# Optimization experiments

Measured on AMD Instinct MI355X. Metric: run time of the kernel, lower is better.

## Reference

```python
import jax, jax.numpy as jnp
import numpy as np

B, Q, K = 4, 1024, 2048
QDIM, MDIM, EDIM, H = 1024, 1024, 1024, 16
HD = EDIM // H

def setup_inputs() -> dict:
    key = jax.random.key(0)
    ks = jax.random.split(key, 7)
    s = lambda d: (1.0 / np.sqrt(d))
    return {
        'query': jax.random.normal(ks[0], (B, Q, QDIM), jnp.float32),
        'memory': jax.random.normal(ks[1], (B, K, MDIM), jnp.float32),
        'bias': jax.random.normal(ks[2], (B, K), jnp.float32),
        'Wq': jax.random.normal(ks[3], (QDIM, EDIM), jnp.float32) * s(QDIM),
        'Wk': jax.random.normal(ks[4], (MDIM, EDIM), jnp.float32) * s(MDIM),
        'Wv': jax.random.normal(ks[5], (MDIM, EDIM), jnp.float32) * s(MDIM),
        'Wo': jax.random.normal(ks[6], (EDIM, EDIM), jnp.float32) * s(EDIM),
    }

def reference(query, memory, bias, Wq, Wk, Wv, Wo):
    scale = HD ** -0.5
    # projections -> [B, H, Q/K, HD]
    q = (query @ Wq).reshape(B, Q, H, HD).transpose(0, 2, 1, 3)
    k = (memory @ Wk).reshape(B, K, H, HD).transpose(0, 2, 1, 3)
    v = (memory @ Wv).reshape(B, K, H, HD).transpose(0, 2, 1, 3)
    scores = jnp.einsum('bhqd,bhkd->bhqk', q, k) * scale
    scores = scores + bias[:, None, None, :]
    weights = jax.nn.softmax(scores, axis=-1)
    out = jnp.einsum('bhqk,bhkd->bhqd', weights, v)
    out = out.transpose(0, 2, 1, 3).reshape(B, Q, EDIM)
    return out @ Wo
```

## Files before the change

### kernel.cpp

```cpp
#include <hip/hip_runtime.h>
#include <cstdint>
#include <cstddef>

typedef unsigned short u16;
typedef __attribute__((ext_vector_type(8))) short bf16x8;
typedef __attribute__((ext_vector_type(4))) short bf16x4;
typedef __attribute__((ext_vector_type(4))) float f32x4;

#define B_  4
#define Q_  1024
#define K_  2048
#define E_  1024
#define H_  16
#define HD_ 64
#define LOG2E 1.4426950408889634f
#define M0_  16.0f

__device__ inline u16 f2bf(float f) {
  union { float f; uint32_t u; } x; x.f = f;
  return (u16)((x.u + 0x7fffu + ((x.u >> 16) & 1u)) >> 16);
}

__device__ inline short bfc(float f) {
  __bf16 h = (__bf16)f;
  return __builtin_bit_cast(short, h);
}

__device__ inline void gload16(const u16* g, u16* l) {
  __builtin_amdgcn_global_load_lds((const __attribute__((address_space(1))) void*)g,
                                   (__attribute__((address_space(3))) void*)l, 16, 0, 0);
}

#define NQ8 (B_ * Q_ * E_ / 8)
#define NM8 (B_ * K_ * E_ / 8)
#define NBI (B_ * K_)
#define NPREP ((NQ8 + NM8 + NBI) / 256)
__global__ __launch_bounds__(256) void prep_all(const float* __restrict__ query,
                                                const float* __restrict__ memory,
                                                const float* __restrict__ bias,
                                                const float* W0, const float* W1,
                                                const float* W2, const float* W3,
                                                u16* __restrict__ qb,
                                                u16* __restrict__ mb,
                                                float* __restrict__ bias2,
                                                u16* T0, u16* T1, u16* T2, u16* T3) {
  __shared__ float t[64][65];
  int bid = blockIdx.x;
  if (bid < NPREP) {
    int i = bid * 256 + threadIdx.x;
    const float* src;
    u16* dst;
    if (i < NQ8) {
      src = query + (size_t)i * 8; dst = qb + (size_t)i * 8;
    } else if (i < NQ8 + NM8) {
      int j = i - NQ8;
      src = memory + (size_t)j * 8; dst = mb + (size_t)j * 8;
    } else {
      int j = i - (NQ8 + NM8);
      if (j < NBI) bias2[j] = bias[j] * LOG2E - M0_;
      return;
    }
    float4 a = *reinterpret_cast<const float4*>(src);
    float4 b = *reinterpret_cast<const float4*>(src + 4);
    union { u16 u[8]; uint4 v; } r;
    r.u[0] = f2bf(a.x); r.u[1] = f2bf(a.y); r.u[2] = f2bf(a.z); r.u[3] = f2bf(a.w);
    r.u[4] = f2bf(b.x); r.u[5] = f2bf(b.y); r.u[6] = f2bf(b.z); r.u[7] = f2bf(b.w);
    *reinterpret_cast<uint4*>(dst) = r.v;
  } else {
    int tb = bid - NPREP;
    int z = tb >> 8, xy = tb & 255;
    const float* W; u16* T;
    switch (z) {
      case 0: W = W0; T = T0; break;
      case 1: W = W1; T = T1; break;
      case 2: W = W2; T = T2; break;
      default: W = W3; T = T3; break;
    }
    int k0 = (xy & 15) * 64, n0 = (xy >> 4) * 64;
    int r = threadIdx.x >> 6, c = threadIdx.x & 63;
#pragma unroll
    for (int i = 0; i < 16; ++i)
      t[r + i * 4][c] = W[(size_t)(k0 + r + i * 4) * E_ + n0 + c];
    __syncthreads();
#pragma unroll
    for (int i = 0; i < 16; ++i)
      T[(size_t)(n0 + r + i * 4) * E_ + k0 + c] = f2bf(t[c][r + i * 4]);
  }
}

template <int MODE>
__device__ __forceinline__ void gemm_body(const u16* __restrict__ A,
                                          const u16* __restrict__ Bt,
                                          void* __restrict__ C,
                                          int M, int N, int Kc, int bx, int by,
                                          u16* As, u16* Bs) {
  const int tid = threadIdx.x;
  const int w = tid >> 6, l = tid & 63;
  const int wr = w >> 1, wc = w & 1;
  const int lr = l & 15, lg = l >> 4;
  const int m0 = bx * 128, n0 = by * 128;
  const int xk = (lr & 7) * 8;

  f32x4 acc[4][4];
#pragma unroll
  for (int mt = 0; mt < 4; ++mt)
#pragma unroll
    for (int nt = 0; nt < 4; ++nt)
      acc[mt][nt] = (f32x4){0.f, 0.f, 0.f, 0.f};

  for (int k0 = 0; k0 < Kc; k0 += 64) {
    __syncthreads();
#pragma unroll
    for (int r = 0; r < 4; ++r) {
      int e = (tid + r * 256) * 8;
      int row = e >> 6, col = e & 63;
      int sc = col ^ ((row & 7) * 8);
      gload16(A  + (size_t)(m0 + row) * Kc + k0 + sc, &As[e]);
      gload16(Bt + (size_t)(n0 + row) * Kc + k0 + sc, &Bs[e]);
    }
    __syncthreads();

#pragma unroll
    for (int ks = 0; ks < 2; ++ks) {
      bf16x8 a[4], b[4];
#pragma unroll
      for (int mt = 0; mt < 4; ++mt) {
        int row = wr * 64 + mt * 16 + lr;
        a[mt] = *reinterpret_cast<const bf16x8*>(&As[row * 64 + ((ks * 32 + lg * 8) ^ xk)]);
      }
#pragma unroll
      for (int nt = 0; nt < 4; ++nt) {
        int row = wc * 64 + nt * 16 + lr;
        b[nt] = *reinterpret_cast<const bf16x8*>(&Bs[row * 64 + ((ks * 32 + lg * 8) ^ xk)]);
      }
#pragma unroll
      for (int mt = 0; mt < 4; ++mt)
#pragma unroll
        for (int nt = 0; nt < 4; ++nt)
          acc[mt][nt] = __builtin_amdgcn_mfma_f32_16x16x32_bf16(a[mt], b[nt], acc[mt][nt], 0, 0, 0);
    }
  }

#pragma unroll
  for (int mt = 0; mt < 4; ++mt) {
#pragma unroll
    for (int nt = 0; nt < 4; ++nt) {
      int col = n0 + wc * 64 + nt * 16 + lr;
#pragma unroll
      for (int j = 0; j < 4; ++j) {
        int row = m0 + wr * 64 + mt * 16 + lg * 4 + j;
        float v = acc[mt][nt][j];
        if (MODE == 0) {
          ((float*)C)[(size_t)row * N + col] = v;
        } else if (MODE == 1) {
          ((u16*)C)[(size_t)row * N + col] = f2bf(v);
        } else if (MODE == 3) {
          ((u16*)C)[(size_t)row * N + col] = f2bf(v * (0.125f * LOG2E));
        } else {
          ((u16*)C)[((size_t)((col >> 11) * 16 + (row >> 6)) * 64 + (row & 63)) * 2048 + (col & 2047)] = f2bf(v);
        }
      }
    }
  }
}

__global__ __launch_bounds__(256) void gemm_out(const u16* __restrict__ A,
                                                const u16* __restrict__ Bt,
                                                void* __restrict__ C,
                                                int M, int N, int Kc) {
  __shared__ u16 As[128 * 64];
  __shared__ u16 Bs[128 * 64];
  int d = blockIdx.x;
  int bid = (d & 7) * 32 + (d >> 3);
  gemm_body<0>(A, Bt, C, M, N, Kc, bid >> 3, bid & 7, As, Bs);
}

__global__ __launch_bounds__(256) void proj_fused(const u16* __restrict__ qb,
                                                  const u16* __restrict__ mb,
                                                  const u16* __restrict__ wqt,
                                                  const u16* __restrict__ wkt,
                                                  const u16* __restrict__ wvt,
                                                  u16* __restrict__ qproj,
                                                  u16* __restrict__ kproj,
                                                  u16* __restrict__ vt) {
  __shared__ u16 As[128 * 64];
  __shared__ u16 Bs[128 * 64];
  int d = blockIdx.x;
  int bid = (d & 7) * 160 + (d >> 3);
  if (bid < 256) {
    gemm_body<3>(qb, wqt, qproj, B_ * Q_, E_, E_, bid >> 3, bid & 7, As, Bs);
  } else if (bid < 768) {
    int i = bid - 256;
    gemm_body<1>(mb, wkt, kproj, B_ * K_, E_, E_, i >> 3, i & 7, As, Bs);
  } else {
    int i = bid - 768;
    gemm_body<2>(wvt, mb, vt, E_, B_ * K_, E_, i & 7, i >> 3, As, Bs);
  }
}

__global__ __launch_bounds__(256, 4) void attn_kernel(const u16* __restrict__ qp,
                                                      const u16* __restrict__ kp,
                                                      const u16* __restrict__ vT,
                                                      const float* __restrict__ bias2,
                                                      u16* __restrict__ out) {
  __shared__ uint4 lds4[2048];
  char* ldsb = (char*)lds4;

  const int blk = blockIdx.x;
  const int hg = blk & 63, qt = blk >> 6;
  const int b = hg >> 4, h = hg & 15;
  const int tid = threadIdx.x;
  const int w = tid >> 6, l = tid & 63;
  const int lr = l & 15, lg = l >> 4;

  bf16x8 qfrag[2];
#pragma unroll
  for (int ks = 0; ks < 2; ++ks)
    qfrag[ks] = *reinterpret_cast<const bf16x8*>(
        qp + (size_t)(b * Q_ + qt * 64 + w * 16 + lr) * E_ + h * 64 + ks * 32 + lg * 8);

  f32x4 O[4];
  f32x4 Osum = (f32x4){0.f, 0.f, 0.f, 0.f};
#pragma unroll
  for (int ht = 0; ht < 4; ++ht) O[ht] = (f32x4){0.f, 0.f, 0.f, 0.f};
  const float* bias_b = bias2 + (size_t)b * K_;
  const u16* kbase = kp + (size_t)b * K_ * E_ + h * 64;
  const u16* vbase = vT + (size_t)(b * H_ + h) * HD_ * K_;

  const bf16x4 ones = {(short)0x3F80, (short)0x3F80, (short)0x3F80, (short)0x3F80};

  const int xk = (lr & 7) * 8;
  int kofs0 = lr * 128 + (((lg * 8) ^ xk) << 1);
  int kofs1 = lr * 128 + ((((32 + lg * 8)) ^ xk) << 1);
  int vofs[4];
#pragma unroll
  for (int ct = 0; ct < 4; ++ct)
    vofs[ct] = 16384 + lr * 128 + ((((ct * 16 + lg * 4)) ^ xk) << 1);

  const int e0 = tid * 8, e1 = e0 + 2048;
  const int r0 = e0 >> 6, r1 = e1 >> 6;
  const int sc0 = (e0 & 63) ^ ((r0 & 7) * 8);
  const int sc1 = (e1 & 63) ^ ((r1 & 7) * 8);

  gload16(kbase + (size_t)r0 * E_ + sc0, (u16*)(ldsb + tid * 16));
  gload16(kbase + (size_t)r1 * E_ + sc1, (u16*)(ldsb + 4096 + tid * 16));
  gload16(vbase + (size_t)r0 * K_ + sc0, (u16*)(ldsb + 16384 + tid * 16));
  gload16(vbase + (size_t)r1 * K_ + sc1, (u16*)(ldsb + 16384 + 4096 + tid * 16));
  __syncthreads();

  const int NT = K_ / 64;
  for (int t = 0; t < NT; ++t) {
    if (t + 1 < NT) {
      const int nb = ((t & 1) ^ 1) * 8192;
      int kk0 = (t + 1) * 64;
      gload16(kbase + (size_t)(kk0 + r0) * E_ + sc0, (u16*)(ldsb + nb + tid * 16));
      gload16(kbase + (size_t)(kk0 + r1) * E_ + sc1, (u16*)(ldsb + nb + 4096 + tid * 16));
      gload16(vbase + (size_t)r0 * K_ + kk0 + sc0, (u16*)(ldsb + 16384 + nb + tid * 16));
      gload16(vbase + (size_t)r1 * K_ + kk0 + sc1, (u16*)(ldsb + 16384 + nb + 4096 + tid * 16));
    }

    const float* bt = bias_b + t * 64;
    f32x4 S[4];
    __builtin_amdgcn_s_setprio(1);
#pragma unroll
    for (int ct = 0; ct < 4; ++ct) {
      bf16x8 kb0 = *reinterpret_cast<const bf16x8*>(ldsb + kofs0 + ct * 2048);
      bf16x8 kb1 = *reinterpret_cast<const bf16x8*>(ldsb + kofs1 + ct * 2048);
      float4 bv = *reinterpret_cast<const float4*>(&bt[ct * 16 + lg * 4]);
      f32x4 s; s[0] = bv.x; s[1] = bv.y; s[2] = bv.z; s[3] = bv.w;
      s = __builtin_amdgcn_mfma_f32_16x16x32_bf16(kb0, qfrag[0], s, 0, 0, 0);
      s = __builtin_amdgcn_mfma_f32_16x16x32_bf16(kb1, qfrag[1], s, 0, 0, 0);
      S[ct] = s;
    }
    __builtin_amdgcn_s_setprio(0);

    bf16x4 pf[4];
#pragma unroll
    for (int ct = 0; ct < 4; ++ct) {
      pf[ct][0] = bfc(exp2f(S[ct][0]));
      pf[ct][1] = bfc(exp2f(S[ct][1]));
      pf[ct][2] = bfc(exp2f(S[ct][2]));
      pf[ct][3] = bfc(exp2f(S[ct][3]));
    }

    __builtin_amdgcn_s_setprio(1);
#pragma unroll
    for (int ct = 0; ct < 4; ++ct) {
#pragma unroll
      for (int ht = 0; ht < 4; ++ht) {
        bf16x4 vb = *reinterpret_cast<const bf16x4*>(ldsb + vofs[ct] + ht * 2048);
        O[ht] = __builtin_amdgcn_mfma_f32_16x16x16bf16_1k(pf[ct], vb, O[ht], 0, 0, 0);
      }
      Osum = __builtin_amdgcn_mfma_f32_16x16x16bf16_1k(pf[ct], ones, Osum, 0, 0, 0);
    }
    __builtin_amdgcn_s_setprio(0);

    kofs0 ^= 8192; kofs1 ^= 8192;
#pragma unroll
    for (int ct = 0; ct < 4; ++ct) vofs[ct] ^= 8192;
    __syncthreads();
  }

#pragma unroll
  for (int j = 0; j < 4; ++j) {
    float inv = 1.f / Osum[j];
    int row = b * Q_ + qt * 64 + w * 16 + lg * 4 + j;
#pragma unroll
    for (int ht = 0; ht < 4; ++ht)
      out[(size_t)row * E_ + h * 64 + ht * 16 + lr] = (u16)bfc(O[ht][j] * inv);
  }
}

extern "C" void kernel_launch(void* const* d_in, const int* in_sizes, int n_in,
                              void* d_out, int out_size, void* d_ws, size_t ws_size,
                              hipStream_t stream) {
  const float* query  = (const float*)d_in[0];
  const float* memory = (const float*)d_in[1];
  const float* bias   = (const float*)d_in[2];
  const float* Wq     = (const float*)d_in[3];
  const float* Wk     = (const float*)d_in[4];
  const float* Wv     = (const float*)d_in[5];
  const float* Wo     = (const float*)d_in[6];
  float* out = (float*)d_out;

  char* p = (char*)d_ws;
  u16* qb    = (u16*)p; p += (size_t)B_ * Q_ * E_ * 2;
  u16* mb    = (u16*)p; p += (size_t)B_ * K_ * E_ * 2;
  u16* wqt   = (u16*)p; p += (size_t)E_ * E_ * 2;
  u16* wkt   = (u16*)p; p += (size_t)E_ * E_ * 2;
  u16* wvt   = (u16*)p; p += (size_t)E_ * E_ * 2;
  u16* wot   = (u16*)p; p += (size_t)E_ * E_ * 2;
  u16* qproj = (u16*)p; p += (size_t)B_ * Q_ * E_ * 2;
  u16* kproj = (u16*)p; p += (size_t)B_ * K_ * E_ * 2;
  u16* vt    = (u16*)p; p += (size_t)B_ * K_ * E_ * 2;
  u16* attn  = (u16*)p; p += (size_t)B_ * Q_ * E_ * 2;
  float* bias2 = (float*)p; p += (size_t)B_ * K_ * 4;

  prep_all<<<NPREP + 1024, 256, 0, stream>>>(query, memory, bias, Wq, Wk, Wv, Wo,
                                             qb, mb, bias2, wqt, wkt, wvt, wot);

  proj_fused<<<1280, 256, 0, stream>>>(qb, mb, wqt, wkt, wvt, qproj, kproj, vt);

  attn_kernel<<<B_ * H_ * (Q_ / 64), 256, 0, stream>>>(qproj, kproj, vt, bias2, attn);

  gemm_out<<<256, 256, 0, stream>>>(attn, wot, out, B_ * Q_, E_, E_);
}
```

Baseline: 164.2 us.

## Double-buffer projection GEMM LDS tiles with K=32 steps and prefetch

The shared GEMM body used by the projection and output kernels is restructured. It now loads A/B tiles of 128x32 into two alternating LDS buffers, prefetching the next K-slice while the MFMAs for the current slice run. A new XOR swizzle suited to 32-wide rows replaces the old one, and s_setprio is raised around the MFMA block. This is meant to hide global-to-LDS latency and remove one of the two barriers per iteration, at the cost of more loop iterations with less MFMA work per barrier.

```diff
diff --git a/kernel.cpp b/kernel.cpp
--- a/kernel.cpp
+++ b/kernel.cpp
@@ -26,7 +26,7 @@
   return __builtin_bit_cast(short, h);
 }
 
-__device__ inline void gload16(const u16* g, u16* l) {
+__device__ inline void gload16(const u16* g, void* l) {
   __builtin_amdgcn_global_load_lds((const __attribute__((address_space(1))) void*)g,
                                    (__attribute__((address_space(3))) void*)l, 16, 0, 0);
 }
@@ -93,13 +93,26 @@
                                           const u16* __restrict__ Bt,
                                           void* __restrict__ C,
                                           int M, int N, int Kc, int bx, int by,
-                                          u16* As, u16* Bs) {
+                                          char* lds) {
   const int tid = threadIdx.x;
   const int w = tid >> 6, l = tid & 63;
   const int wr = w >> 1, wc = w & 1;
   const int lr = l & 15, lg = l >> 4;
   const int m0 = bx * 128, n0 = by * 128;
-  const int xk = (lr & 7) * 8;
+
+  const int e0g = tid * 8, e1g = e0g + 2048;
+  const int row0 = e0g >> 5, row1 = e1g >> 5;
+  const int lc0 = ((((e0g & 31) >> 3) ^ ((row0 >> 1) & 3)) * 8);
+  const int lc1 = ((((e1g & 31) >> 3) ^ ((row1 >> 1) & 3)) * 8);
+  const u16* Ar0 = A  + (size_t)(m0 + row0) * Kc + lc0;
+  const u16* Ar1 = A  + (size_t)(m0 + row1) * Kc + lc1;
+  const u16* Br0 = Bt + (size_t)(n0 + row0) * Kc + lc0;
+  const u16* Br1 = Bt + (size_t)(n0 + row1) * Kc + lc1;
+  const int d0 = tid * 16, d1 = d0 + 4096;
+
+  const int ck = (lg ^ ((lr >> 1) & 3)) * 16;
+  int aofs = (wr * 64 + lr) * 64 + ck;
+  int bofs = 16384 + (wc * 64 + lr) * 64 + ck;
 
   f32x4 acc[4][4];
 #pragma unroll
@@ -108,37 +121,40 @@
     for (int nt = 0; nt < 4; ++nt)
       acc[mt][nt] = (f32x4){0.f, 0.f, 0.f, 0.f};
 
-  for (int k0 = 0; k0 < Kc; k0 += 64) {
+  gload16(Ar0, lds + d0);
+  gload16(Ar1, lds + d1);
+  gload16(Br0, lds + 16384 + d0);
+  gload16(Br1, lds + 16384 + d1);
+  __syncthreads();
+
+  const int NI = Kc >> 5;
+  for (int ki = 0; ki < NI; ++ki) {
+    if (ki + 1 < NI) {
+      const int nb = ((ki & 1) ^ 1) * 8192;
+      const int kk = (ki + 1) * 32;
+      gload16(Ar0 + kk, lds + nb + d0);
+      gload16(Ar1 + kk, lds + nb + d1);
+      gload16(Br0 + kk, lds + 16384 + nb + d0);
+      gload16(Br1 + kk, lds + 16384 + nb + d1);
+    }
+
+    bf16x8 a[4], b[4];
+#pragma unroll
+    for (int mt = 0; mt < 4; ++mt)
+      a[mt] = *reinterpret_cast<const bf16x8*>(lds + aofs + mt * 1024);
+#pragma unroll
+    for (int nt = 0; nt < 4; ++nt)
+      b[nt] = *reinterpret_cast<const bf16x8*>(lds + bofs + nt * 1024);
+    __builtin_amdgcn_s_setprio(1);
+#pragma unroll
+    for (int mt = 0; mt < 4; ++mt)
+#pragma unroll
+      for (int nt = 0; nt < 4; ++nt)
+        acc[mt][nt] = __builtin_amdgcn_mfma_f32_16x16x32_bf16(a[mt], b[nt], acc[mt][nt], 0, 0, 0);
+    __builtin_amdgcn_s_setprio(0);
+
+    aofs ^= 8192; bofs ^= 8192;
     __syncthreads();
-#pragma unroll
-    for (int r = 0; r < 4; ++r) {
-      int e = (tid + r * 256) * 8;
-      int row = e >> 6, col = e & 63;
-      int sc = col ^ ((row & 7) * 8);
-      gload16(A  + (size_t)(m0 + row) * Kc + k0 + sc, &As[e]);
-      gload16(Bt + (size_t)(n0 + row) * Kc + k0 + sc, &Bs[e]);
-    }
-    __syncthreads();
-
-#pragma unroll
-    for (int ks = 0; ks < 2; ++ks) {
-      bf16x8 a[4], b[4];
-#pragma unroll
-      for (int mt = 0; mt < 4; ++mt) {
-        int row = wr * 64 + mt * 16 + lr;
-        a[mt] = *reinterpret_cast<const bf16x8*>(&As[row * 64 + ((ks * 32 + lg * 8) ^ xk)]);
-      }
-#pragma unroll
-      for (int nt = 0; nt < 4; ++nt) {
-        int row = wc * 64 + nt * 16 + lr;
-        b[nt] = *reinterpret_cast<const bf16x8*>(&Bs[row * 64 + ((ks * 32 + lg * 8) ^ xk)]);
-      }
-#pragma unroll
-      for (int mt = 0; mt < 4; ++mt)
-#pragma unroll
-        for (int nt = 0; nt < 4; ++nt)
-          acc[mt][nt] = __builtin_amdgcn_mfma_f32_16x16x32_bf16(a[mt], b[nt], acc[mt][nt], 0, 0, 0);
-    }
   }
 
 #pragma unroll
@@ -168,11 +184,10 @@
                                                 const u16* __restrict__ Bt,
                                                 void* __restrict__ C,
                                                 int M, int N, int Kc) {
-  __shared__ u16 As[128 * 64];
-  __shared__ u16 Bs[128 * 64];
+  __shared__ uint4 lds4[2048];
   int d = blockIdx.x;
   int bid = (d & 7) * 32 + (d >> 3);
-  gemm_body<0>(A, Bt, C, M, N, Kc, bid >> 3, bid & 7, As, Bs);
+  gemm_body<0>(A, Bt, C, M, N, Kc, bid >> 3, bid & 7, (char*)lds4);
 }
 
 __global__ __launch_bounds__(256) void proj_fused(const u16* __restrict__ qb,
@@ -183,18 +198,18 @@
                                                   u16* __restrict__ qproj,
                                                   u16* __restrict__ kproj,
                                                   u16* __restrict__ vt) {
-  __shared__ u16 As[128 * 64];
-  __shared__ u16 Bs[128 * 64];
+  __shared__ uint4 lds4[2048];
+  char* lds = (char*)lds4;
   int d = blockIdx.x;
   int bid = (d & 7) * 160 + (d >> 3);
   if (bid < 256) {
-    gemm_body<3>(qb, wqt, qproj, B_ * Q_, E_, E_, bid >> 3, bid & 7, As, Bs);
+    gemm_body<3>(qb, wqt, qproj, B_ * Q_, E_, E_, bid >> 3, bid & 7, lds);
   } else if (bid < 768) {
     int i = bid - 256;
-    gemm_body<1>(mb, wkt, kproj, B_ * K_, E_, E_, i >> 3, i & 7, As, Bs);
+    gemm_body<1>(mb, wkt, kproj, B_ * K_, E_, E_, i >> 3, i & 7, lds);
   } else {
     int i = bid - 768;
-    gemm_body<2>(wvt, mb, vt, E_, B_ * K_, E_, i & 7, i >> 3, As, Bs);
+    gemm_body<2>(wvt, mb, vt, E_, B_ * K_, E_, i & 7, i >> 3, lds);
   }
 }
 
@@ -242,10 +257,10 @@
   const int sc0 = (e0 & 63) ^ ((r0 & 7) * 8);
   const int sc1 = (e1 & 63) ^ ((r1 & 7) * 8);
 
-  gload16(kbase + (size_t)r0 * E_ + sc0, (u16*)(ldsb + tid * 16));
-  gload16(kbase + (size_t)r1 * E_ + sc1, (u16*)(ldsb + 4096 + tid * 16));
-  gload16(vbase + (size_t)r0 * K_ + sc0, (u16*)(ldsb + 16384 + tid * 16));
-  gload16(vbase + (size_t)r1 * K_ + sc1, (u16*)(ldsb + 16384 + 4096 + tid * 16));
+  gload16(kbase + (size_t)r0 * E_ + sc0, ldsb + tid * 16);
+  gload16(kbase + (size_t)r1 * E_ + sc1, ldsb + 4096 + tid * 16);
+  gload16(vbase + (size_t)r0 * K_ + sc0, ldsb + 16384 + tid * 16);
+  gload16(vbase + (size_t)r1 * K_ + sc1, ldsb + 16384 + 4096 + tid * 16);
   __syncthreads();
 
   const int NT = K_ / 64;
@@ -253,10 +268,10 @@
     if (t + 1 < NT) {
       const int nb = ((t & 1) ^ 1) * 8192;
       int kk0 = (t + 1) * 64;
-      gload16(kbase + (size_t)(kk0 + r0) * E_ + sc0, (u16*)(ldsb + nb + tid * 16));
-      gload16(kbase + (size_t)(kk0 + r1) * E_ + sc1, (u16*)(ldsb + nb + 4096 + tid * 16));
-      gload16(vbase + (size_t)r0 * K_ + kk0 + sc0, (u16*)(ldsb + 16384 + nb + tid * 16));
-      gload16(vbase + (size_t)r1 * K_ + kk0 + sc1, (u16*)(ldsb + 16384 + nb + 4096 + tid * 16));
+      gload16(kbase + (size_t)(kk0 + r0) * E_ + sc0, ldsb + nb + tid * 16);
+      gload16(kbase + (size_t)(kk0 + r1) * E_ + sc1, ldsb + nb + 4096 + tid * 16);
+      gload16(vbase + (size_t)r0 * K_ + kk0 + sc0, ldsb + 16384 + nb + tid * 16);
+      gload16(vbase + (size_t)r1 * K_ + kk0 + sc1, ldsb + 16384 + nb + 4096 + tid * 16);
     }
 
     const float* bt = bias_b + t * 64;
```

Result: faster. 152.4 us (-7.2%).
